# Kernel optimization log

Measured on AMD Instinct MI355X. Metric: run time of the kernel, lower is better.

Reference implementation:

```python
import jax, jax.numpy as jnp
import numpy as np

B, M, R = 2, 2048, 256
H, DH = 16, 64
ROPE_THETA = 10000.0


def setup_inputs() -> dict:
    key = jax.random.key(0)
    ks = jax.random.split(key, 9)
    d = H * DH
    inp = {
        "Pq": jax.random.normal(ks[0], (B, M, R), jnp.float32),
        "Pk": jax.random.normal(ks[1], (B, M, R), jnp.float32),
        "Pv": jax.random.normal(ks[2], (B, M, R), jnp.float32),
        "Vq": jax.random.normal(ks[3], (R, d), jnp.float32) / np.sqrt(R),
        "Vk": jax.random.normal(ks[4], (R, d), jnp.float32) / np.sqrt(R),
        "Vv": jax.random.normal(ks[5], (R, d), jnp.float32) / np.sqrt(R),
        "bq": jax.random.normal(ks[6], (d,), jnp.float32),
        "bk": jax.random.normal(ks[7], (d,), jnp.float32),
        "bv": jax.random.normal(ks[8], (d,), jnp.float32),
        "attention_mask": jnp.ones((B, M), jnp.int32),
        "position_ids": jnp.tile(jnp.arange(M, dtype=jnp.int32), (B, 1)),
    }
    return inp


def _rope_cos_sin(position_ids):
    # half-half RoPE tables; kernel only reads the first half of cos/sin
    inv_freq = 1.0 / (ROPE_THETA ** (jnp.arange(0, DH, 2, dtype=jnp.float32) / DH))
    freqs = position_ids.astype(jnp.float32)[:, :, None] * inv_freq[None, None, :]  # [B,M,DH/2]
    return jnp.cos(freqs)[:, None], jnp.sin(freqs)[:, None]  # [B,1,M,DH/2]


def _heads(P, V, b):
    # low-rank reconstruction: [B,M,R] @ [R,H*DH] + [H*DH] -> [B,H,M,DH]
    x = jnp.einsum('bmr,rd->bmd', P, V) + b
    return x.reshape(x.shape[0], x.shape[1], H, DH).transpose(0, 2, 1, 3)


def _rotate(x, cos, sin):
    x0, x1 = x[..., :DH // 2], x[..., DH // 2:]
    return jnp.concatenate([x0 * cos - x1 * sin, x0 * sin + x1 * cos], axis=-1)


def reference(Pq, Pk, Pv, Vq, Vk, Vv, bq, bk, bv, attention_mask, position_ids):
    cos, sin = _rope_cos_sin(position_ids)
    q = _rotate(_heads(Pq, Vq, bq), cos, sin)  # [B,H,M,DH]
    k = _rotate(_heads(Pk, Vk, bk), cos, sin)
    v = _heads(Pv, Vv, bv)
    scale = 1.0 / jnp.sqrt(jnp.float32(DH))
    scores = jnp.einsum('bhmd,bhnd->bhmn', q, k) * scale
    keep = attention_mask.astype(bool)[:, None, None, :]
    scores = jnp.where(keep, scores, -jnp.inf)
    # online-softmax equivalent with all-masked-row zeroing (matches kernel)
    mx = jnp.max(scores, axis=-1, keepdims=True)
    safe_mx = jnp.where(jnp.isfinite(mx), mx, 0.0)
    p = jnp.exp(scores - safe_mx)
    l = jnp.sum(p, axis=-1, keepdims=True)
    out = jnp.einsum('bhmn,bhnd->bhmd', p, v) / jnp.where(l > 0, l, 1.0)
    out = jnp.where(l > 0, out, 0.0)
    return out  # [B,H,M,DH]
```

## Files before the change

### kernel.cpp

```cpp
#include <hip/hip_runtime.h>
#include <cstdint>
#include <cstddef>

#define Bc 2
#define Mc 2048
#define Rc 256
#define Hc 16
#define DHc 64
#define Dc (Hc * DHc)
#define NKT (Mc / 64)

typedef __attribute__((ext_vector_type(8))) short short8;
typedef __attribute__((ext_vector_type(4))) float float4v;
typedef __attribute__((ext_vector_type(4))) unsigned short ushort4v;
typedef __attribute__((ext_vector_type(4))) unsigned int uint4v;

#if __has_builtin(__builtin_amdgcn_exp2f)
#define EXPFN(x) __builtin_amdgcn_exp2f(x)
#define QSCALE 0.18033688f
#define MADD_KEEP (-28.8539008f)
#else
#define EXPFN(x) __expf(x)
#define QSCALE 0.125f
#define MADD_KEEP (-20.0f)
#endif

__device__ inline unsigned short f2bf(float f) {
    union { float f; uint32_t u; } v;
    v.f = f;
    uint32_t r = v.u + 0x7fffu + ((v.u >> 16) & 1u);
    return (unsigned short)(r >> 16);
}

__device__ inline int swz(int row, int chunk) {
    return row * 128 + ((chunk ^ (row & 7)) << 4);
}

__global__ __launch_bounds__(256)
void convP(const float* __restrict__ P0, const float* __restrict__ P1,
           const float* __restrict__ P2, unsigned short* __restrict__ Pb)
{
    const int mat = blockIdx.y;
    const float* src = mat == 0 ? P0 : (mat == 1 ? P1 : P2);
    size_t idx = ((size_t)blockIdx.x * 256 + threadIdx.x) * 8;
    float4 f0 = *(const float4*)&src[idx];
    float4 f1 = *(const float4*)&src[idx + 4];
    ushort4v a = { f2bf(f0.x), f2bf(f0.y), f2bf(f0.z), f2bf(f0.w) };
    ushort4v c = { f2bf(f1.x), f2bf(f1.y), f2bf(f1.z), f2bf(f1.w) };
    unsigned short* dst = Pb + (size_t)mat * Bc * Mc * Rc + idx;
    *(ushort4v*)dst = a;
    *(ushort4v*)(dst + 4) = c;
}

__global__ __launch_bounds__(256)
void transpose_v(const float* __restrict__ V0, const float* __restrict__ V1,
                 const float* __restrict__ V2, unsigned short* __restrict__ Vt)
{
    const int mat = blockIdx.z;
    const float* src = mat == 0 ? V0 : (mat == 1 ? V1 : V2);
    const int d  = blockIdx.x * 256 + threadIdx.x;
    const int kg = blockIdx.y;
    short8 v;
    #pragma unroll
    for (int j = 0; j < 8; ++j)
        v[j] = (short)f2bf(src[(size_t)(kg * 8 + j) * Dc + d]);
    *(short8*)&Vt[((size_t)mat * Dc + d) * Rc + kg * 8] = v;
}

__global__ __launch_bounds__(256)
void rope_madd(const int* __restrict__ pos_ids, const int* __restrict__ mask,
               float2* __restrict__ ropetab, float* __restrict__ maddf)
{
    int row = blockIdx.x * 8 + (threadIdx.x >> 5);
    int j = threadIdx.x & 31;
    float inv = __expf(-0.28782314f * (float)j);
    float ang = (float)pos_ids[row] * inv;
    ropetab[(size_t)row * 32 + j] = make_float2(__cosf(ang), __sinf(ang));
    if (j == 0) maddf[row] = mask[row] ? MADD_KEEP : -1e30f;
}

__global__ __launch_bounds__(256, 2)
void proj_kernel(const unsigned short* __restrict__ Pb,
                 const unsigned short* __restrict__ Vtp,
                 const float* __restrict__ bq, const float* __restrict__ bk,
                 const float* __restrict__ bv,
                 const float2* __restrict__ ropetab,
                 unsigned short* __restrict__ Qb, unsigned short* __restrict__ Kb,
                 unsigned short* __restrict__ Vta)
{
    __shared__ __align__(16) unsigned char AtB[128 * 128];
    __shared__ __align__(16) unsigned char BtB[128 * 128];

    const int tid = threadIdx.x;
    const int z = blockIdx.z, mat = z >> 1, b = z & 1;
    const int m0 = blockIdx.x * 128, d0 = blockIdx.y * 128;
    const int w = tid >> 6, lane = tid & 63, col = lane & 15, quad = lane >> 4;
    const int mh = w & 1, dh2 = w >> 1;

    const unsigned short* Pg = Pb + ((size_t)mat * Bc + b) * Mc * Rc + (size_t)m0 * Rc;
    const unsigned short* Vg = Vtp + (size_t)mat * Dc * Rc + (size_t)d0 * Rc;

    const int srow = tid >> 1, sc0 = (tid & 1) * 4;

    float4v acc[4][4] = {};

    for (int kc = 0; kc < 4; ++kc) {
        uint4v ar[4], br[4];
        #pragma unroll
        for (int i = 0; i < 4; ++i) {
            ar[i] = *(const uint4v*)&Pg[(size_t)srow * Rc + kc * 64 + (sc0 + i) * 8];
            br[i] = *(const uint4v*)&Vg[(size_t)srow * Rc + kc * 64 + (sc0 + i) * 8];
        }
        __syncthreads();
        #pragma unroll
        for (int i = 0; i < 4; ++i) {
            *(uint4v*)(AtB + swz(srow, sc0 + i)) = ar[i];
            *(uint4v*)(BtB + swz(srow, sc0 + i)) = br[i];
        }
        __syncthreads();

        #pragma unroll
        for (int kk = 0; kk < 2; ++kk) {
            short8 af[4], bf[4];
            #pragma unroll
            for (int mt = 0; mt < 4; ++mt)
                af[mt] = *(const short8*)(AtB + swz(mh * 64 + mt * 16 + col, kk * 4 + quad));
            #pragma unroll
            for (int dt = 0; dt < 4; ++dt)
                bf[dt] = *(const short8*)(BtB + swz(dh2 * 64 + dt * 16 + col, kk * 4 + quad));
            #pragma unroll
            for (int mt = 0; mt < 4; ++mt)
                #pragma unroll
                for (int dt = 0; dt < 4; ++dt)
                    acc[mt][dt] = __builtin_amdgcn_mfma_f32_16x16x32_bf16(
                        af[mt], bf[dt], acc[mt][dt], 0, 0, 0);
        }
    }

    const int head = (d0 + dh2 * 64) >> 6;
    const int bh = b * Hc + head;

    if (mat < 2) {
        const float* bias = mat == 0 ? bq : bk;
        unsigned short* outp = mat == 0 ? Qb : Kb;
        const float oscale = mat == 0 ? QSCALE : 1.0f;
        float b00 = bias[head * 64 + col],      b01 = bias[head * 64 + 16 + col];
        float b10 = bias[head * 64 + 32 + col], b11 = bias[head * 64 + 48 + col];
        #pragma unroll
        for (int mt = 0; mt < 4; ++mt)
            #pragma unroll
            for (int r = 0; r < 4; ++r) {
                int m = m0 + mh * 64 + mt * 16 + quad * 4 + r;
                float2 cs0 = ropetab[((size_t)b * Mc + m) * 32 + col];
                float2 cs1 = ropetab[((size_t)b * Mc + m) * 32 + 16 + col];
                float x00 = acc[mt][0][r] + b00, x10 = acc[mt][2][r] + b10;
                float x01 = acc[mt][1][r] + b01, x11 = acc[mt][3][r] + b11;
                unsigned short* og = outp + ((size_t)bh * Mc + m) * DHc;
                og[col]      = f2bf((x00 * cs0.x - x10 * cs0.y) * oscale);
                og[32 + col] = f2bf((x00 * cs0.y + x10 * cs0.x) * oscale);
                og[16 + col] = f2bf((x01 * cs1.x - x11 * cs1.y) * oscale);
                og[48 + col] = f2bf((x01 * cs1.y + x11 * cs1.x) * oscale);
            }
    } else {
        #pragma unroll
        for (int dt = 0; dt < 4; ++dt) {
            int d = d0 + dh2 * 64 + dt * 16 + col;
            float bb = bv[d];
            int dh = d & 63;
            #pragma unroll
            for (int mt = 0; mt < 4; ++mt) {
                ushort4v pv;
                #pragma unroll
                for (int r = 0; r < 4; ++r) pv[r] = f2bf(acc[mt][dt][r] + bb);
                size_t base = ((size_t)bh * DHc + dh) * Mc + m0 + mh * 64 + mt * 16 + quad * 4;
                *(ushort4v*)&Vta[base] = pv;
            }
        }
    }
}

__global__ __launch_bounds__(256, 2)
void attn_kernel(const unsigned short* __restrict__ Qb,
                 const unsigned short* __restrict__ Kb,
                 const unsigned short* __restrict__ Vt,
                 const float* __restrict__ maddf,
                 float* __restrict__ out)
{
    __shared__ __align__(16) unsigned char KsB[64 * 128];
    __shared__ __align__(16) unsigned char VsB[64 * 128];
    __shared__ __align__(16) unsigned short Ps[4][32][72];

    const int tid = threadIdx.x;
    const int q0 = blockIdx.x * 128;
    const int bh = blockIdx.y;
    const int b  = bh >> 4;
    const int w = tid >> 6, lane = tid & 63, col = lane & 15, quad = lane >> 4;

    short8 qf[2][2];
    #pragma unroll
    for (int qs = 0; qs < 2; ++qs) {
        const unsigned short* Qg =
            Qb + ((size_t)bh * Mc + q0 + w * 32 + qs * 16 + col) * DHc + quad * 8;
        qf[qs][0] = *(const short8*)Qg;
        qf[qs][1] = *(const short8*)(Qg + 32);
    }

    const int srow = tid >> 3, sc = tid & 7;
    const int dst0 = swz(srow, sc), dst1 = swz(srow + 32, sc);
    const unsigned short* Kg = Kb + (size_t)bh * Mc * DHc;
    const unsigned short* Vg = Vt + (size_t)bh * DHc * Mc;
    const float* mdp = maddf + b * Mc;

    uint4v kr0 = *(const uint4v*)&Kg[(size_t)srow * DHc + sc * 8];
    uint4v kr1 = *(const uint4v*)&Kg[(size_t)(srow + 32) * DHc + sc * 8];
    uint4v vr0 = *(const uint4v*)&Vg[(size_t)srow * Mc + sc * 8];
    uint4v vr1 = *(const uint4v*)&Vg[(size_t)(srow + 32) * Mc + sc * 8];

    float lsum[2] = {0.0f, 0.0f};
    float4v acc_o[2][4] = {};

    for (int kt = 0; kt < NKT; ++kt) {
        __syncthreads();
        *(uint4v*)(KsB + dst0) = kr0; *(uint4v*)(KsB + dst1) = kr1;
        *(uint4v*)(VsB + dst0) = vr0; *(uint4v*)(VsB + dst1) = vr1;
        __syncthreads();

        if (kt + 1 < NKT) {
            const unsigned short* Kn = Kg + (size_t)(kt + 1) * 64 * DHc;
            kr0 = *(const uint4v*)&Kn[(size_t)srow * DHc + sc * 8];
            kr1 = *(const uint4v*)&Kn[(size_t)(srow + 32) * DHc + sc * 8];
            vr0 = *(const uint4v*)&Vg[(size_t)srow * Mc + (kt + 1) * 64 + sc * 8];
            vr1 = *(const uint4v*)&Vg[(size_t)(srow + 32) * Mc + (kt + 1) * 64 + sc * 8];
        }

        float4 md[4];
        #pragma unroll
        for (int ks = 0; ks < 4; ++ks)
            md[ks] = *(const float4*)&mdp[kt * 64 + ks * 16 + quad * 4];

        float4v sacc[4][2] = {};
        #pragma unroll
        for (int ks = 0; ks < 4; ++ks) {
            short8 a0 = *(const short8*)(KsB + swz(ks * 16 + col, quad));
            short8 a1 = *(const short8*)(KsB + swz(ks * 16 + col, 4 + quad));
            #pragma unroll
            for (int qs = 0; qs < 2; ++qs) {
                sacc[ks][qs] = __builtin_amdgcn_mfma_f32_16x16x32_bf16(
                    a0, qf[qs][0], sacc[ks][qs], 0, 0, 0);
                sacc[ks][qs] = __builtin_amdgcn_mfma_f32_16x16x32_bf16(
                    a1, qf[qs][1], sacc[ks][qs], 0, 0, 0);
            }
        }

        #pragma unroll
        for (int ks = 0; ks < 4; ++ks) {
            const float* mdk = (const float*)&md[ks];
            #pragma unroll
            for (int qs = 0; qs < 2; ++qs) {
                ushort4v pw;
                #pragma unroll
                for (int r = 0; r < 4; ++r) {
                    float p = EXPFN(sacc[ks][qs][r] + mdk[r]);
                    lsum[qs] += p;
                    union { float f; uint32_t u; } cv; cv.f = p;
                    pw[r] = (unsigned short)((cv.u + 0x8000u) >> 16);
                }
                *(ushort4v*)&Ps[w][qs * 16 + col][ks * 16 + quad * 4] = pw;
            }
        }

        #pragma unroll
        for (int kk = 0; kk < 2; ++kk) {
            short8 pa0 = *(const short8*)&Ps[w][col][kk * 32 + quad * 8];
            short8 pa1 = *(const short8*)&Ps[w][16 + col][kk * 32 + quad * 8];
            #pragma unroll
            for (int ds = 0; ds < 4; ++ds) {
                short8 vb = *(const short8*)(VsB + swz(ds * 16 + col, kk * 4 + quad));
                acc_o[0][ds] = __builtin_amdgcn_mfma_f32_16x16x32_bf16(
                    pa0, vb, acc_o[0][ds], 0, 0, 0);
                acc_o[1][ds] = __builtin_amdgcn_mfma_f32_16x16x32_bf16(
                    pa1, vb, acc_o[1][ds], 0, 0, 0);
            }
        }
    }

    #pragma unroll
    for (int qs = 0; qs < 2; ++qs) {
        lsum[qs] += __shfl_xor(lsum[qs], 16);
        lsum[qs] += __shfl_xor(lsum[qs], 32);
    }

    #pragma unroll
    for (int qs = 0; qs < 2; ++qs)
        #pragma unroll
        for (int r = 0; r < 4; ++r) {
            float lr = __shfl(lsum[qs], quad * 4 + r);
            float inv = (lr > 0.0f) ? 1.0f / lr : 0.0f;
            int m = q0 + w * 32 + qs * 16 + quad * 4 + r;
            float* og = out + ((size_t)bh * Mc + m) * DHc;
            #pragma unroll
            for (int ds = 0; ds < 4; ++ds)
                og[ds * 16 + col] = acc_o[qs][ds][r] * inv;
        }
}

extern "C" void kernel_launch(void* const* d_in, const int* in_sizes, int n_in,
                              void* d_out, int out_size, void* d_ws, size_t ws_size,
                              hipStream_t stream) {
    const float* Pq = (const float*)d_in[0];
    const float* Pk = (const float*)d_in[1];
    const float* Pv = (const float*)d_in[2];
    const float* Vq = (const float*)d_in[3];
    const float* Vk = (const float*)d_in[4];
    const float* Vv = (const float*)d_in[5];
    const float* bq = (const float*)d_in[6];
    const float* bk = (const float*)d_in[7];
    const float* bv = (const float*)d_in[8];
    const int*   am = (const int*)d_in[9];
    const int*   pid = (const int*)d_in[10];
    float* out = (float*)d_out;

    const size_t n_el = (size_t)Bc * Hc * Mc * DHc;
    unsigned short* Qb  = (unsigned short*)d_ws;
    unsigned short* Kb  = Qb + n_el;
    unsigned short* Vta = Kb + n_el;
    unsigned short* Pb  = Vta + n_el;
    unsigned short* Vtp = Pb + (size_t)3 * Bc * Mc * Rc;
    float2* ropetab = (float2*)(Vtp + (size_t)3 * Dc * Rc);
    float*  maddf   = (float*)(ropetab + (size_t)Bc * Mc * 32);

    dim3 blk(256);
    convP<<<dim3((Bc * Mc * Rc) / 8 / 256, 3), blk, 0, stream>>>(Pq, Pk, Pv, Pb);
    transpose_v<<<dim3(Dc / 256, Rc / 8, 3), blk, 0, stream>>>(Vq, Vk, Vv, Vtp);
    rope_madd<<<dim3(Bc * Mc / 8), blk, 0, stream>>>(pid, am, ropetab, maddf);

    proj_kernel<<<dim3(Mc / 128, Dc / 128, 6), blk, 0, stream>>>(
        Pb, Vtp, bq, bk, bv, ropetab, Qb, Kb, Vta);

    attn_kernel<<<dim3(Mc / 128, Bc * Hc), blk, 0, stream>>>(Qb, Kb, Vta, maddf, out);
}
```

Baseline: 167.4 us.

## Fuse input conversion into projection and split attention keys across two blocks

Removes the separate fp32-to-bf16 conversion, V transpose and rope/mask table kernels. The projection now reads fp32 inputs directly, converts and transposes them while staging into LDS, and computes RoPE cos/sin inline. Attention is split into two halves along the key dimension, which doubles the grid for better CU occupancy. Partial outputs and row sums are written out and merged by a new combine kernel. The cost is extra fp32 global traffic for the partial outputs and scattered 2-byte LDS stores for the transposed B tile.

```diff
diff --git a/kernel.cpp b/kernel.cpp
--- a/kernel.cpp
+++ b/kernel.cpp
@@ -9,10 +9,13 @@
 #define DHc 64
 #define Dc (Hc * DHc)
 #define NKT (Mc / 64)
+#define NSPLIT 2
+#define NKT2 (NKT / NSPLIT)
 
 typedef __attribute__((ext_vector_type(8))) short short8;
 typedef __attribute__((ext_vector_type(4))) float float4v;
 typedef __attribute__((ext_vector_type(4))) unsigned short ushort4v;
+typedef __attribute__((ext_vector_type(8))) unsigned short ushort8v;
 typedef __attribute__((ext_vector_type(4))) unsigned int uint4v;
 
 #if __has_builtin(__builtin_amdgcn_exp2f)
@@ -37,54 +40,13 @@
 }
 
 __global__ __launch_bounds__(256)
-void convP(const float* __restrict__ P0, const float* __restrict__ P1,
-           const float* __restrict__ P2, unsigned short* __restrict__ Pb)
-{
-    const int mat = blockIdx.y;
-    const float* src = mat == 0 ? P0 : (mat == 1 ? P1 : P2);
-    size_t idx = ((size_t)blockIdx.x * 256 + threadIdx.x) * 8;
-    float4 f0 = *(const float4*)&src[idx];
-    float4 f1 = *(const float4*)&src[idx + 4];
-    ushort4v a = { f2bf(f0.x), f2bf(f0.y), f2bf(f0.z), f2bf(f0.w) };
-    ushort4v c = { f2bf(f1.x), f2bf(f1.y), f2bf(f1.z), f2bf(f1.w) };
-    unsigned short* dst = Pb + (size_t)mat * Bc * Mc * Rc + idx;
-    *(ushort4v*)dst = a;
-    *(ushort4v*)(dst + 4) = c;
-}
-
-__global__ __launch_bounds__(256)
-void transpose_v(const float* __restrict__ V0, const float* __restrict__ V1,
-                 const float* __restrict__ V2, unsigned short* __restrict__ Vt)
-{
-    const int mat = blockIdx.z;
-    const float* src = mat == 0 ? V0 : (mat == 1 ? V1 : V2);
-    const int d  = blockIdx.x * 256 + threadIdx.x;
-    const int kg = blockIdx.y;
-    short8 v;
-    #pragma unroll
-    for (int j = 0; j < 8; ++j)
-        v[j] = (short)f2bf(src[(size_t)(kg * 8 + j) * Dc + d]);
-    *(short8*)&Vt[((size_t)mat * Dc + d) * Rc + kg * 8] = v;
-}
-
-__global__ __launch_bounds__(256)
-void rope_madd(const int* __restrict__ pos_ids, const int* __restrict__ mask,
-               float2* __restrict__ ropetab, float* __restrict__ maddf)
-{
-    int row = blockIdx.x * 8 + (threadIdx.x >> 5);
-    int j = threadIdx.x & 31;
-    float inv = __expf(-0.28782314f * (float)j);
-    float ang = (float)pos_ids[row] * inv;
-    ropetab[(size_t)row * 32 + j] = make_float2(__cosf(ang), __sinf(ang));
-    if (j == 0) maddf[row] = mask[row] ? MADD_KEEP : -1e30f;
-}
-
-__global__ __launch_bounds__(256, 2)
-void proj_kernel(const unsigned short* __restrict__ Pb,
-                 const unsigned short* __restrict__ Vtp,
+void proj_kernel(const float* __restrict__ Pq, const float* __restrict__ Pk,
+                 const float* __restrict__ Pv,
+                 const float* __restrict__ Vq, const float* __restrict__ Vk,
+                 const float* __restrict__ Vv,
                  const float* __restrict__ bq, const float* __restrict__ bk,
                  const float* __restrict__ bv,
-                 const float2* __restrict__ ropetab,
+                 const int* __restrict__ pos_ids,
                  unsigned short* __restrict__ Qb, unsigned short* __restrict__ Kb,
                  unsigned short* __restrict__ Vta)
 {
@@ -97,43 +59,62 @@
     const int w = tid >> 6, lane = tid & 63, col = lane & 15, quad = lane >> 4;
     const int mh = w & 1, dh2 = w >> 1;
 
-    const unsigned short* Pg = Pb + ((size_t)mat * Bc + b) * Mc * Rc + (size_t)m0 * Rc;
-    const unsigned short* Vg = Vtp + (size_t)mat * Dc * Rc + (size_t)d0 * Rc;
-
-    const int srow = tid >> 1, sc0 = (tid & 1) * 4;
+    const float* P  = mat == 0 ? Pq : (mat == 1 ? Pk : Pv);
+    const float* Vm = mat == 0 ? Vq : (mat == 1 ? Vk : Vv);
+    const float* Pg = P + ((size_t)b * Mc + m0) * Rc;
+
+    const int arow = tid >> 1, ac0 = (tid & 1) * 4;
+    const int bkr = tid >> 2, bd = (tid & 3) * 32;
 
     float4v acc[4][4] = {};
 
     for (int kc = 0; kc < 4; ++kc) {
-        uint4v ar[4], br[4];
+        float4 af[8], bf4[8];
+        #pragma unroll
+        for (int i = 0; i < 8; ++i)
+            af[i] = *(const float4*)&Pg[(size_t)arow * Rc + kc * 64 + (tid & 1) * 32 + i * 4];
+        #pragma unroll
+        for (int i = 0; i < 8; ++i)
+            bf4[i] = *(const float4*)&Vm[(size_t)(kc * 64 + bkr) * Dc + d0 + bd + i * 4];
+        ushort8v ua[4];
         #pragma unroll
         for (int i = 0; i < 4; ++i) {
-            ar[i] = *(const uint4v*)&Pg[(size_t)srow * Rc + kc * 64 + (sc0 + i) * 8];
-            br[i] = *(const uint4v*)&Vg[(size_t)srow * Rc + kc * 64 + (sc0 + i) * 8];
+            float4 f0 = af[2 * i], f1 = af[2 * i + 1];
+            ushort8v u = { f2bf(f0.x), f2bf(f0.y), f2bf(f0.z), f2bf(f0.w),
+                           f2bf(f1.x), f2bf(f1.y), f2bf(f1.z), f2bf(f1.w) };
+            ua[i] = u;
         }
         __syncthreads();
         #pragma unroll
-        for (int i = 0; i < 4; ++i) {
-            *(uint4v*)(AtB + swz(srow, sc0 + i)) = ar[i];
-            *(uint4v*)(BtB + swz(srow, sc0 + i)) = br[i];
+        for (int i = 0; i < 4; ++i)
+            *(ushort8v*)(AtB + swz(arow, ac0 + i)) = ua[i];
+        #pragma unroll
+        for (int i = 0; i < 8; ++i) {
+            const float* fp = (const float*)&bf4[i];
+            #pragma unroll
+            for (int c = 0; c < 4; ++c) {
+                int d = bd + i * 4 + c;
+                *(unsigned short*)(BtB + d * 128 + (((bkr >> 3) ^ (d & 7)) << 4)
+                                   + (bkr & 7) * 2) = f2bf(fp[c]);
+            }
         }
         __syncthreads();
 
         #pragma unroll
         for (int kk = 0; kk < 2; ++kk) {
-            short8 af[4], bf[4];
+            short8 afr[4], bfr[4];
             #pragma unroll
             for (int mt = 0; mt < 4; ++mt)
-                af[mt] = *(const short8*)(AtB + swz(mh * 64 + mt * 16 + col, kk * 4 + quad));
+                afr[mt] = *(const short8*)(AtB + swz(mh * 64 + mt * 16 + col, kk * 4 + quad));
             #pragma unroll
             for (int dt = 0; dt < 4; ++dt)
-                bf[dt] = *(const short8*)(BtB + swz(dh2 * 64 + dt * 16 + col, kk * 4 + quad));
+                bfr[dt] = *(const short8*)(BtB + swz(dh2 * 64 + dt * 16 + col, kk * 4 + quad));
             #pragma unroll
             for (int mt = 0; mt < 4; ++mt)
                 #pragma unroll
                 for (int dt = 0; dt < 4; ++dt)
                     acc[mt][dt] = __builtin_amdgcn_mfma_f32_16x16x32_bf16(
-                        af[mt], bf[dt], acc[mt][dt], 0, 0, 0);
+                        afr[mt], bfr[dt], acc[mt][dt], 0, 0, 0);
         }
     }
 
@@ -146,20 +127,24 @@
         const float oscale = mat == 0 ? QSCALE : 1.0f;
         float b00 = bias[head * 64 + col],      b01 = bias[head * 64 + 16 + col];
         float b10 = bias[head * 64 + 32 + col], b11 = bias[head * 64 + 48 + col];
+        float if0 = __expf(-0.28782314f * (float)col);
+        float if1 = __expf(-0.28782314f * (float)(col + 16));
         #pragma unroll
         for (int mt = 0; mt < 4; ++mt)
             #pragma unroll
             for (int r = 0; r < 4; ++r) {
                 int m = m0 + mh * 64 + mt * 16 + quad * 4 + r;
-                float2 cs0 = ropetab[((size_t)b * Mc + m) * 32 + col];
-                float2 cs1 = ropetab[((size_t)b * Mc + m) * 32 + 16 + col];
+                float pos = (float)pos_ids[b * Mc + m];
+                float a0 = pos * if0, a1 = pos * if1;
+                float cs0 = __cosf(a0), sn0 = __sinf(a0);
+                float cs1 = __cosf(a1), sn1 = __sinf(a1);
                 float x00 = acc[mt][0][r] + b00, x10 = acc[mt][2][r] + b10;
                 float x01 = acc[mt][1][r] + b01, x11 = acc[mt][3][r] + b11;
                 unsigned short* og = outp + ((size_t)bh * Mc + m) * DHc;
-                og[col]      = f2bf((x00 * cs0.x - x10 * cs0.y) * oscale);
-                og[32 + col] = f2bf((x00 * cs0.y + x10 * cs0.x) * oscale);
-                og[16 + col] = f2bf((x01 * cs1.x - x11 * cs1.y) * oscale);
-                og[48 + col] = f2bf((x01 * cs1.y + x11 * cs1.x) * oscale);
+                og[col]      = f2bf((x00 * cs0 - x10 * sn0) * oscale);
+                og[32 + col] = f2bf((x00 * sn0 + x10 * cs0) * oscale);
+                og[16 + col] = f2bf((x01 * cs1 - x11 * sn1) * oscale);
+                og[48 + col] = f2bf((x01 * sn1 + x11 * cs1) * oscale);
             }
     } else {
         #pragma unroll
@@ -183,8 +168,10 @@
 void attn_kernel(const unsigned short* __restrict__ Qb,
                  const unsigned short* __restrict__ Kb,
                  const unsigned short* __restrict__ Vt,
-                 const float* __restrict__ maddf,
-                 float* __restrict__ out)
+                 const int* __restrict__ mask,
+                 float* __restrict__ O0,
+                 float* __restrict__ O1,
+                 float* __restrict__ lpart)
 {
     __shared__ __align__(16) unsigned char KsB[64 * 128];
     __shared__ __align__(16) unsigned char VsB[64 * 128];
@@ -194,6 +181,7 @@
     const int q0 = blockIdx.x * 128;
     const int bh = blockIdx.y;
     const int b  = bh >> 4;
+    const int s  = blockIdx.z;
     const int w = tid >> 6, lane = tid & 63, col = lane & 15, quad = lane >> 4;
 
     short8 qf[2][2];
@@ -207,9 +195,9 @@
 
     const int srow = tid >> 3, sc = tid & 7;
     const int dst0 = swz(srow, sc), dst1 = swz(srow + 32, sc);
-    const unsigned short* Kg = Kb + (size_t)bh * Mc * DHc;
-    const unsigned short* Vg = Vt + (size_t)bh * DHc * Mc;
-    const float* mdp = maddf + b * Mc;
+    const unsigned short* Kg = Kb + (size_t)bh * Mc * DHc + (size_t)s * (Mc / 2) * DHc;
+    const unsigned short* Vg = Vt + (size_t)bh * DHc * Mc + s * (Mc / 2);
+    const int* mp = mask + b * Mc + s * (Mc / 2);
 
     uint4v kr0 = *(const uint4v*)&Kg[(size_t)srow * DHc + sc * 8];
     uint4v kr1 = *(const uint4v*)&Kg[(size_t)(srow + 32) * DHc + sc * 8];
@@ -219,13 +207,13 @@
     float lsum[2] = {0.0f, 0.0f};
     float4v acc_o[2][4] = {};
 
-    for (int kt = 0; kt < NKT; ++kt) {
+    for (int kt = 0; kt < NKT2; ++kt) {
         __syncthreads();
         *(uint4v*)(KsB + dst0) = kr0; *(uint4v*)(KsB + dst1) = kr1;
         *(uint4v*)(VsB + dst0) = vr0; *(uint4v*)(VsB + dst1) = vr1;
         __syncthreads();
 
-        if (kt + 1 < NKT) {
+        if (kt + 1 < NKT2) {
             const unsigned short* Kn = Kg + (size_t)(kt + 1) * 64 * DHc;
             kr0 = *(const uint4v*)&Kn[(size_t)srow * DHc + sc * 8];
             kr1 = *(const uint4v*)&Kn[(size_t)(srow + 32) * DHc + sc * 8];
@@ -233,10 +221,10 @@
             vr1 = *(const uint4v*)&Vg[(size_t)(srow + 32) * Mc + (kt + 1) * 64 + sc * 8];
         }
 
-        float4 md[4];
+        int4 mv[4];
         #pragma unroll
         for (int ks = 0; ks < 4; ++ks)
-            md[ks] = *(const float4*)&mdp[kt * 64 + ks * 16 + quad * 4];
+            mv[ks] = *(const int4*)&mp[kt * 64 + ks * 16 + quad * 4];
 
         float4v sacc[4][2] = {};
         #pragma unroll
@@ -254,13 +242,14 @@
 
         #pragma unroll
         for (int ks = 0; ks < 4; ++ks) {
-            const float* mdk = (const float*)&md[ks];
+            const int* mi = (const int*)&mv[ks];
             #pragma unroll
             for (int qs = 0; qs < 2; ++qs) {
                 ushort4v pw;
                 #pragma unroll
                 for (int r = 0; r < 4; ++r) {
-                    float p = EXPFN(sacc[ks][qs][r] + mdk[r]);
+                    float madd = mi[r] ? MADD_KEEP : -1e30f;
+                    float p = EXPFN(sacc[ks][qs][r] + madd);
                     lsum[qs] += p;
                     union { float f; uint32_t u; } cv; cv.f = p;
                     pw[r] = (unsigned short)((cv.u + 0x8000u) >> 16);
@@ -290,18 +279,39 @@
         lsum[qs] += __shfl_xor(lsum[qs], 32);
     }
 
+    float* Opart = (s == 0) ? O0 : O1;
     #pragma unroll
     for (int qs = 0; qs < 2; ++qs)
         #pragma unroll
         for (int r = 0; r < 4; ++r) {
-            float lr = __shfl(lsum[qs], quad * 4 + r);
-            float inv = (lr > 0.0f) ? 1.0f / lr : 0.0f;
             int m = q0 + w * 32 + qs * 16 + quad * 4 + r;
-            float* og = out + ((size_t)bh * Mc + m) * DHc;
+            float* og = Opart + ((size_t)bh * Mc + m) * DHc;
             #pragma unroll
             for (int ds = 0; ds < 4; ++ds)
-                og[ds * 16 + col] = acc_o[qs][ds][r] * inv;
-        }
+                og[ds * 16 + col] = acc_o[qs][ds][r];
+        }
+    if (quad == 0) {
+        #pragma unroll
+        for (int qs = 0; qs < 2; ++qs)
+            lpart[((size_t)s * Bc * Hc + bh) * Mc + q0 + w * 32 + qs * 16 + col] = lsum[qs];
+    }
+}
+
+__global__ __launch_bounds__(256)
+void combine_kernel(float* __restrict__ out, const float* __restrict__ O1,
+                    const float* __restrict__ lpart)
+{
+    size_t i = ((size_t)blockIdx.x * 256 + threadIdx.x) * 4;
+    int row = (int)(i >> 6);
+    float sl = lpart[row] + lpart[(size_t)Bc * Hc * Mc + row];
+    float inv = (sl > 0.0f) ? 1.0f / sl : 0.0f;
+    float4 a = *(const float4*)&out[i];
+    const float4 bb = *(const float4*)&O1[i];
+    a.x = (a.x + bb.x) * inv;
+    a.y = (a.y + bb.y) * inv;
+    a.z = (a.z + bb.z) * inv;
+    a.w = (a.w + bb.w) * inv;
+    *(float4*)&out[i] = a;
 }
 
 extern "C" void kernel_launch(void* const* d_in, const int* in_sizes, int n_in,
@@ -324,18 +334,15 @@
     unsigned short* Qb  = (unsigned short*)d_ws;
     unsigned short* Kb  = Qb + n_el;
     unsigned short* Vta = Kb + n_el;
-    unsigned short* Pb  = Vta + n_el;
-    unsigned short* Vtp = Pb + (size_t)3 * Bc * Mc * Rc;
-    float2* ropetab = (float2*)(Vtp + (size_t)3 * Dc * Rc);
-    float*  maddf   = (float*)(ropetab + (size_t)Bc * Mc * 32);
+    float* O1    = (float*)(Vta + n_el);
+    float* lpart = O1 + n_el;
 
     dim3 blk(256);
-    convP<<<dim3((Bc * Mc * Rc) / 8 / 256, 3), blk, 0, stream>>>(Pq, Pk, Pv, Pb);
-    transpose_v<<<dim3(Dc / 256, Rc / 8, 3), blk, 0, stream>>>(Vq, Vk, Vv, Vtp);
-    rope_madd<<<dim3(Bc * Mc / 8), blk, 0, stream>>>(pid, am, ropetab, maddf);
-
     proj_kernel<<<dim3(Mc / 128, Dc / 128, 6), blk, 0, stream>>>(
-        Pb, Vtp, bq, bk, bv, ropetab, Qb, Kb, Vta);
-
-    attn_kernel<<<dim3(Mc / 128, Bc * Hc), blk, 0, stream>>>(Qb, Kb, Vta, maddf, out);
-}
+        Pq, Pk, Pv, Vq, Vk, Vv, bq, bk, bv, pid, Qb, Kb, Vta);
+
+    attn_kernel<<<dim3(Mc / 128, Bc * Hc, NSPLIT), blk, 0, stream>>>(
+        Qb, Kb, Vta, am, out, O1, lpart);
+
+    combine_kernel<<<dim3((unsigned)(n_el / 1024)), blk, 0, stream>>>(out, O1, lpart);
+}
```

New measurement: 180.2 us. +7.7%, slower.
